# Kernel optimization log

Hardware: AMD Instinct MI355X
Metric: run time of the kernel (lower is better)

## Reference

```python
import jax, jax.numpy as jnp
import numpy as np
import math
from jax import lax

ALPHA = 2.0          # surrogate.ATan(alpha=2.0)
TAU = 2.0
BASE_THR = 1.0
ADAPT = 0.1          # adaptation_strength
TARGET_RATE = 0.1
DECAY = math.exp(-1.0 / TAU)
N_HEAD = 4

@jax.custom_vjp
def atan_spike(x):
    # forward: Heaviside; backward: ATan surrogate gradient
    return (x >= 0).astype(x.dtype)

def _atan_fwd(x):
    return atan_spike(x), x

def _atan_bwd(x, g):
    return (g * (ALPHA / 2.0) / (1.0 + (math.pi / 2.0 * ALPHA * x) ** 2),)

atan_spike.defvjp(_atan_fwd, _atan_bwd)

def lif_step(x, v_mem, thr):
    # AdaptiveLIFNeuron.forward
    v_pot = v_mem * DECAY + x
    spike = atan_spike(v_pot - thr)
    sd = lax.stop_gradient(spike)
    v_new = v_pot * (1.0 - sd)                               # spike.detach()
    thr_new = thr + ADAPT * (sd.mean(axis=(0, 1)) - TARGET_RATE)  # no_grad buffer update
    return spike, v_new, thr_new

def setup_inputs() -> dict:
    key = jax.random.key(0)
    ks = jax.random.split(key, 12)
    B, T, S, dm, ds = 4, 96, 128, 512, 256
    W = 0.02  # scale weights so per-step activations stay numerically sane
    return {
        'x':  jax.random.normal(ks[0], (B, T, S, dm), jnp.float32),
        'A':  jax.random.normal(ks[1], (ds, ds), jnp.float32) * W,
        'C':  jax.random.normal(ks[2], (dm, ds), jnp.float32) * W,
        'D':  jax.random.normal(ks[3], (dm, dm), jnp.float32) * W,
        'Wq': jax.random.normal(ks[4], (ds, ds), jnp.float32) * W,
        'bq': jax.random.normal(ks[5], (ds,), jnp.float32) * W,
        'Wk': jax.random.normal(ks[6], (ds, dm), jnp.float32) * W,
        'bk': jax.random.normal(ks[7], (ds,), jnp.float32) * W,
        'Wv': jax.random.normal(ks[8], (ds, dm), jnp.float32) * W,
        'bv': jax.random.normal(ks[9], (ds,), jnp.float32) * W,
        'Wo': jax.random.normal(ks[10], (ds, ds), jnp.float32) * W,
        'bo': jax.random.normal(ks[11], (ds,), jnp.float32) * W,
    }

def _forward(x, A, C, D, Wq, bq, Wk, bk, Wv, bv, Wo, bo):
    B, T, S, dm = x.shape
    ds = A.shape[0]
    H = N_HEAD
    dh = ds // H
    BS = B * S
    scale = 1.0 / math.sqrt(dh)

    h0 = jnp.zeros((B, S, ds), x.dtype)
    sv0 = jnp.zeros((B, S, ds), x.dtype)
    ov0 = jnp.zeros((B, S, dm), x.dtype)
    ts0 = jnp.full((ds,), BASE_THR, x.dtype)
    to0 = jnp.full((dm,), BASE_THR, x.dtype)

    def step(carry, x_t):
        h, sv, ov, ts, to = carry
        st = h @ A.T  # state transition [B,S,ds]

        def active(_):
            q = (h @ Wq.T + bq).reshape(BS, H, dh)
            k = (x_t @ Wk.T + bk).reshape(BS, H, dh)
            v = (x_t @ Wv.T + bv).reshape(BS, H, dh)
            # attention over all B*S tokens jointly, per head: [H, BS, BS]
            w = jax.nn.softmax(jnp.einsum('qhd,khd->hqk', q, k) * scale, axis=-1)
            av = jnp.einsum('hqk,khd->qhd', w, v).reshape(B, S, ds)
            gi = av @ Wo.T + bo
            h2, sv2, ts2 = lif_step(st + gi, sv, ts)
            out_up = h2 @ C.T + x_t @ D.T
            os_, ov2, to2 = lif_step(out_up, ov, to)
            return (h2, sv2, ov2, ts2, to2, os_)

        def inactive(_):
            h2, sv2, ts2 = lif_step(st, sv, ts)
            return (h2, sv2, ov, ts2, to, jnp.zeros_like(x_t))

        h2, sv2, ov2, ts2, to2, os_ = lax.cond(jnp.any(x_t > 0), active, inactive, None)
        return (h2, sv2, ov2, ts2, to2), os_

    xs = jnp.swapaxes(x, 0, 1)  # [T,B,S,dm]
    _, outs = lax.scan(step, (h0, sv0, ov0, ts0, to0), xs)
    return jnp.swapaxes(outs, 0, 1)  # [B,T,S,dm]

def reference(x, A, C, D, Wq, bq, Wk, bk, Wv, bv, Wo, bo):
    return _forward(x, A, C, D, Wq, bq, Wk, bk, Wv, bv, Wo, bo)
```

## Files before the change

### kernel.cpp

```cpp
#include <hip/hip_runtime.h>
#include <math.h>

#define TT   96
#define SSS  128
#define DMM  512
#define DSS  256
#define BSS  512
#define NBLK 128
#define NTHR 1024
#define DECAYF 0.6065306597126334f
#define SMEM_BYTES 135712

static constexpr size_t OFS_K      = 0;
static constexpr size_t OFS_V      = 12582912;
static constexpr size_t OFS_XD     = 25165824;
static constexpr size_t OFS_AT     = 50331648;
static constexpr size_t OFS_WQT    = 50397184;
static constexpr size_t OFS_WOT    = 50462720;
static constexpr size_t OFS_CT     = 50528256;
static constexpr size_t OFS_TPART  = 50659328;
static constexpr size_t OFS_TOPART = 50671616;
static constexpr size_t OFS_FLAGS  = 50696192;
static constexpr size_t OFS_BAR    = 50696320;
static constexpr size_t WS_FLOATS  = 50696384;

#define L_PART 0
#define L_SW   16640
#define L_SH   24960
#define L_SSV  25984
#define L_SST  27008
#define L_SQV  28032
#define L_SAV  29056
#define L_SOV  30080
#define L_STS  32128
#define L_STO  32384
#define L_ACT  32896
#define L_NACT 33920

__device__ __forceinline__ void gridbar(int* bar, int* bok) {
  __syncthreads();
  if (threadIdx.x == 0) {
    if (*bok) {
      __threadfence();
      int* cnt = bar;
      int* gen = bar + 32;
      int g = __hip_atomic_load(gen, __ATOMIC_ACQUIRE, __HIP_MEMORY_SCOPE_AGENT);
      int a = __hip_atomic_fetch_add(cnt, 1, __ATOMIC_ACQ_REL, __HIP_MEMORY_SCOPE_AGENT);
      if (a == NBLK - 1) {
        __hip_atomic_store(cnt, 0, __ATOMIC_RELAXED, __HIP_MEMORY_SCOPE_AGENT);
        __hip_atomic_fetch_add(gen, 1, __ATOMIC_ACQ_REL, __HIP_MEMORY_SCOPE_AGENT);
      } else {
        int spin = 0;
        while (__hip_atomic_load(gen, __ATOMIC_ACQUIRE, __HIP_MEMORY_SCOPE_AGENT) == g) {
          __builtin_amdgcn_s_sleep(8);
          if (++spin > (1 << 22)) { *bok = 0; break; }
        }
      }
      __threadfence();
    }
  }
  __syncthreads();
}

extern "C" __global__ void __launch_bounds__(256)
zfill_kernel(float* __restrict__ out, int n) {
  int i = blockIdx.x * 256 + threadIdx.x;
  if (i < n) out[i] = 0.f;
}

extern "C" __global__ void __launch_bounds__(256)
flags_kernel(const float* __restrict__ x, int* __restrict__ flags) {
  __shared__ int f;
  if (threadIdx.x == 0) f = 0;
  __syncthreads();
  int t = blockIdx.x;
  int any = 0;
  for (int b = 0; b < 4; ++b) {
    const float4* base = (const float4*)(x + ((size_t)(b * TT + t) * SSS) * DMM);
    for (int i = threadIdx.x; i < 16384; i += 256) {
      float4 v = base[i];
      any |= (v.x > 0.f) | (v.y > 0.f) | (v.z > 0.f) | (v.w > 0.f);
    }
  }
  if (any) atomicOr(&f, 1);
  __syncthreads();
  if (threadIdx.x == 0) flags[t] = f;
}

extern "C" __global__ void __launch_bounds__(256)
tr_kernel(const float* __restrict__ A, const float* __restrict__ Wq,
          const float* __restrict__ Wo, const float* __restrict__ C,
          float* __restrict__ ws) {
  __shared__ float tile[32][33];
  int b = blockIdx.x;
  const float* src; float* dst; int RS, CS, tb;
  if (b < 64)       { src = A;  dst = ws + OFS_AT;  RS = 256; CS = 256; tb = b; }
  else if (b < 128) { src = Wq; dst = ws + OFS_WQT; RS = 256; CS = 256; tb = b - 64; }
  else if (b < 192) { src = Wo; dst = ws + OFS_WOT; RS = 256; CS = 256; tb = b - 128; }
  else              { src = C;  dst = ws + OFS_CT;  RS = 512; CS = 256; tb = b - 192; }
  int tpr = CS / 32;
  int trr = tb / tpr, tcc = tb % tpr;
  int r0 = trr * 32, c0 = tcc * 32;
  int tx = threadIdx.x & 31, ty = threadIdx.x >> 5;
  #pragma unroll
  for (int j = 0; j < 4; ++j)
    tile[ty + j * 8][tx] = src[(size_t)(r0 + ty + j * 8) * CS + c0 + tx];
  __syncthreads();
  #pragma unroll
  for (int j = 0; j < 4; ++j)
    dst[(size_t)(c0 + ty + j * 8) * RS + r0 + tx] = tile[tx][ty + j * 8];
}

extern "C" __global__ void __launch_bounds__(256)
pre_kernel(const float* __restrict__ x,
           const float* __restrict__ Wk, const float* __restrict__ bk,
           const float* __restrict__ Wv, const float* __restrict__ bv,
           const float* __restrict__ D,  float* __restrict__ ws) {
  __shared__ float As[32 * 68];
  __shared__ float Bs[32 * 68];
  int bid = blockIdx.x;
  int nt = bid & 15, mt = bid >> 4;
  int row0 = mt * 64, col0 = nt * 64;
  int tid = threadIdx.x;
  int trd = tid & 15, tc = tid >> 4;
  float acc[4][4] = {};
  for (int kk = 0; kk < 512; kk += 32) {
    __syncthreads();
    { int m = tid >> 2, ks = (tid & 3) * 8;
      const float* src = x + (size_t)(row0 + m) * 512 + kk + ks;
      float4 a = *(const float4*)(src);
      float4 b = *(const float4*)(src + 4);
      As[(ks + 0) * 68 + m] = a.x; As[(ks + 1) * 68 + m] = a.y;
      As[(ks + 2) * 68 + m] = a.z; As[(ks + 3) * 68 + m] = a.w;
      As[(ks + 4) * 68 + m] = b.x; As[(ks + 5) * 68 + m] = b.y;
      As[(ks + 6) * 68 + m] = b.z; As[(ks + 7) * 68 + m] = b.w; }
    { int n = tid >> 2, ks = (tid & 3) * 8;
      int gc = col0 + n;
      const float* wr = (gc < 256) ? (Wk + (size_t)gc * 512)
                      : (gc < 512) ? (Wv + (size_t)(gc - 256) * 512)
                                   : (D  + (size_t)(gc - 512) * 512);
      const float* src = wr + kk + ks;
      float4 a = *(const float4*)(src);
      float4 b = *(const float4*)(src + 4);
      Bs[(ks + 0) * 68 + n] = a.x; Bs[(ks + 1) * 68 + n] = a.y;
      Bs[(ks + 2) * 68 + n] = a.z; Bs[(ks + 3) * 68 + n] = a.w;
      Bs[(ks + 4) * 68 + n] = b.x; Bs[(ks + 5) * 68 + n] = b.y;
      Bs[(ks + 6) * 68 + n] = b.z; Bs[(ks + 7) * 68 + n] = b.w; }
    __syncthreads();
    #pragma unroll 8
    for (int k = 0; k < 32; ++k) {
      float4 a4 = *(const float4*)(As + k * 68 + trd * 4);
      float4 b4 = *(const float4*)(Bs + k * 68 + tc * 4);
      float am[4] = {a4.x, a4.y, a4.z, a4.w};
      float bn[4] = {b4.x, b4.y, b4.z, b4.w};
      #pragma unroll
      for (int i = 0; i < 4; ++i)
        #pragma unroll
        for (int j = 0; j < 4; ++j)
          acc[i][j] = fmaf(am[i], bn[j], acc[i][j]);
    }
  }
  for (int i = 0; i < 4; ++i) {
    int g = row0 + trd * 4 + i;
    int b = g / 12288, r1 = g % 12288;
    int t_ = r1 / 128, s_ = r1 % 128;
    size_t drow = (size_t)t_ * BSS + b * SSS + s_;
    int gc0 = col0 + tc * 4;
    float4 o = make_float4(acc[i][0], acc[i][1], acc[i][2], acc[i][3]);
    if (gc0 < 256) {
      o.x += bk[gc0]; o.y += bk[gc0 + 1]; o.z += bk[gc0 + 2]; o.w += bk[gc0 + 3];
      *(float4*)(ws + OFS_K + drow * DSS + gc0) = o;
    } else if (gc0 < 512) {
      int c = gc0 - 256;
      o.x += bv[c]; o.y += bv[c + 1]; o.z += bv[c + 2]; o.w += bv[c + 3];
      *(float4*)(ws + OFS_V + drow * DSS + c) = o;
    } else {
      *(float4*)(ws + OFS_XD + drow * DMM + (gc0 - 512)) = o;
    }
  }
}

extern "C" __global__ void __launch_bounds__(NTHR, 4)
seq_kernel(const float* __restrict__ bq, const float* __restrict__ bo,
           float* __restrict__ ws, float* __restrict__ out) {
  extern __shared__ float sm[];
  float* part = sm + L_PART;
  float* sw   = sm + L_SW;
  float* sh   = sm + L_SH;
  float* ssv  = sm + L_SSV;
  float* sst  = sm + L_SST;
  float* sqv  = sm + L_SQV;
  float* sav  = sm + L_SAV;
  float* sou  = sm + L_SQV;
  float* sov  = sm + L_SOV;
  float* sts  = sm + L_STS;
  float* sto  = sm + L_STO;
  int*   acts = (int*)(sm + L_ACT);
  int*   nact = (int*)(sm + L_NACT);
  int*   bok  = nact + 7;

  const float* At  = ws + OFS_AT;
  const float* Wqt = ws + OFS_WQT;
  const float* Wot = ws + OFS_WOT;
  const float* Ct  = ws + OFS_CT;
  const float* XD  = ws + OFS_XD;
  float* tpart  = ws + OFS_TPART;
  float* topart = ws + OFS_TOPART;
  const int* flags = (const int*)(ws + OFS_FLAGS);
  int* bar = (int*)(ws + OFS_BAR);

  const int tid = threadIdx.x;
  const int bid = blockIdx.x;

  sh[tid] = 0.f;
  ssv[tid] = 0.f;
  sov[tid] = 0.f; sov[1024 + tid] = 0.f;
  if (tid < 256) sts[tid] = 1.f;
  if (tid < 512) sto[tid] = 1.f;
  if (tid == 0) *bok = 1;
  { size_t g0 = (size_t)bid * NTHR + tid;
    for (size_t i = g0; i < (size_t)36864; i += (size_t)NBLK * NTHR)
      tpart[i] = 0.f; }
  gridbar(bar, bok);

  for (int t = 0; t < TT; ++t) {
    const int fl = flags[t];
    const int tb3 = t % 3;
    const float* Kt = ws + OFS_K + (size_t)t * BSS * DSS;
    const float* Vt = ws + OFS_V + (size_t)t * BSS * DSS;

    if (tid < 256) {
      int r = tid >> 6, lane = tid & 63;
      int base = 0;
      for (int seg = 0; seg < 4; ++seg) {
        int k = seg * 64 + lane;
        bool p = sh[r * 256 + k] > 0.5f;
        unsigned long long m = __ballot(p);
        int pre = __popcll(m & ((1ull << lane) - 1ull));
        if (p) acts[r * 256 + base + pre] = k;
        base += __popcll(m);
      }
      if (lane == 0) nact[r] = base;
    }
    __syncthreads();

    {
      int r = tid >> 8, c = tid & 255;
      int n = nact[r];
      const int* al = acts + r * 256;
      float aS = 0.f, aQ = 0.f;
      if (fl) {
        for (int i = 0; i < n; ++i) {
          int k = al[i];
          aS += At[(size_t)k * 256 + c];
          aQ += Wqt[(size_t)k * 256 + c];
        }
        sqv[r * 256 + c] = aQ + bq[c];
      } else {
        for (int i = 0; i < n; ++i) aS += At[(size_t)(al[i]) * 256 + c];
      }
      sst[r * 256 + c] = aS;
    }
    __syncthreads();

    if (fl) {
      int kl = tid >> 5, dsg = tid & 31;
      float4 qa[4], qb[4];
      #pragma unroll
      for (int r = 0; r < 4; ++r) {
        qa[r] = *(const float4*)(sqv + r * 256 + dsg * 8);
        qb[r] = *(const float4*)(sqv + r * 256 + dsg * 8 + 4);
      }
      for (int kb = 0; kb < 16; ++kb) {
        int key = kb * 32 + kl;
        const float4* kp = (const float4*)(Kt + (size_t)key * 256 + dsg * 8);
        float4 k0 = kp[0], k1 = kp[1];
        float p[4];
        #pragma unroll
        for (int r = 0; r < 4; ++r) {
          float s = 0.f;
          s = fmaf(k0.x, qa[r].x, s); s = fmaf(k0.y, qa[r].y, s);
          s = fmaf(k0.z, qa[r].z, s); s = fmaf(k0.w, qa[r].w, s);
          s = fmaf(k1.x, qb[r].x, s); s = fmaf(k1.y, qb[r].y, s);
          s = fmaf(k1.z, qb[r].z, s); s = fmaf(k1.w, qb[r].w, s);
          p[r] = s;
        }
        *(float4*)(part + (size_t)(kl * 33 + dsg) * 4) = make_float4(p[0], p[1], p[2], p[3]);
        __syncthreads();
        if (tid < 512) {
          int r2 = tid >> 7, hd = (tid >> 5) & 3, kl2 = tid & 31;
          float s = 0.f;
          #pragma unroll
          for (int d8 = 0; d8 < 8; ++d8)
            s += part[(size_t)(kl2 * 33 + hd * 8 + d8) * 4 + r2];
          sw[(r2 * 4 + hd) * 520 + kb * 32 + kl2] = s * 0.125f;
        }
        __syncthreads();
      }

      {
        int w = tid >> 6, lane = tid & 63;
        float* row = sw + w * 520;
        float4 v0 = ((const float4*)row)[lane * 2];
        float4 v1 = ((const float4*)row)[lane * 2 + 1];
        float m = fmaxf(fmaxf(fmaxf(v0.x, v0.y), fmaxf(v0.z, v0.w)),
                        fmaxf(fmaxf(v1.x, v1.y), fmaxf(v1.z, v1.w)));
        for (int o = 32; o > 0; o >>= 1) m = fmaxf(m, __shfl_xor(m, o));
        v0.x = expf(v0.x - m); v0.y = expf(v0.y - m); v0.z = expf(v0.z - m); v0.w = expf(v0.w - m);
        v1.x = expf(v1.x - m); v1.y = expf(v1.y - m); v1.z = expf(v1.z - m); v1.w = expf(v1.w - m);
        float s = v0.x + v0.y + v0.z + v0.w + v1.x + v1.y + v1.z + v1.w;
        for (int o = 32; o > 0; o >>= 1) s += __shfl_xor(s, o);
        float inv = 1.f / s;
        v0.x *= inv; v0.y *= inv; v0.z *= inv; v0.w *= inv;
        v1.x *= inv; v1.y *= inv; v1.z *= inv; v1.w *= inv;
        ((float4*)row)[lane * 2] = v0; ((float4*)row)[lane * 2 + 1] = v1;
      }
      __syncthreads();

      {
        int kg = tid >> 6, dq = tid & 63;
        int hd = dq >> 4;
        float4 acc[4];
        #pragma unroll
        for (int r = 0; r < 4; ++r) acc[r] = make_float4(0.f, 0.f, 0.f, 0.f);
        for (int kb = 0; kb < 8; ++kb) {
          #pragma unroll
          for (int i = 0; i < 4; ++i) {
            int key = kb * 64 + kg * 4 + i;
            float4 v = *(const float4*)(Vt + (size_t)key * 256 + dq * 4);
            #pragma unroll
            for (int r = 0; r < 4; ++r) {
              float wv = sw[(r * 4 + hd) * 520 + key];
              acc[r].x = fmaf(wv, v.x, acc[r].x);
              acc[r].y = fmaf(wv, v.y, acc[r].y);
              acc[r].z = fmaf(wv, v.z, acc[r].z);
              acc[r].w = fmaf(wv, v.w, acc[r].w);
            }
          }
        }
        #pragma unroll
        for (int r = 0; r < 4; ++r)
          *(float4*)(part + (size_t)((kg * 4 + r) * 64 + dq) * 4) = acc[r];
      }
      __syncthreads();
      {
        int row = tid >> 8, dd = tid & 255;
        float s = 0.f;
        #pragma unroll
        for (int kg = 0; kg < 16; ++kg)
          s += part[(size_t)kg * 1024 + row * 256 + dd];
        sav[row * 256 + dd] = s;
      }
      __syncthreads();
    }

    {
      int r = tid >> 8, c = tid & 255;
      float gi = 0.f;
      if (fl) {
        int ks4 = (tid >> 6) & 3, cq = tid & 63;
        float4 a = make_float4(0.f, 0.f, 0.f, 0.f);
        const float* avr = sav + r * 256;
        for (int k = ks4 * 64; k < ks4 * 64 + 64; ++k) {
          float avv = avr[k];
          float4 wo = *(const float4*)(Wot + (size_t)k * 256 + cq * 4);
          a.x = fmaf(avv, wo.x, a.x); a.y = fmaf(avv, wo.y, a.y);
          a.z = fmaf(avv, wo.z, a.z); a.w = fmaf(avv, wo.w, a.w);
        }
        *(float4*)(part + (size_t)((r * 4 + ks4) * 64 + cq) * 4) = a;
        __syncthreads();
        gi = (((part[(size_t)(r * 4 + 0) * 256 + c]
              + part[(size_t)(r * 4 + 1) * 256 + c])
              + part[(size_t)(r * 4 + 2) * 256 + c])
              + part[(size_t)(r * 4 + 3) * 256 + c]) + bo[c];
      }
      float in1 = sst[r * 256 + c] + gi;
      float vp = ssv[r * 256 + c] * DECAYF + in1;
      float sp = (vp >= sts[c]) ? 1.f : 0.f;
      ssv[r * 256 + c] = vp * (1.f - sp);
      sh[r * 256 + c] = sp;
    }
    __syncthreads();
    if (tid < 256) {
      float s = sh[tid] + sh[256 + tid] + sh[512 + tid] + sh[768 + tid];
      atomicAdd(tpart + ((size_t)tb3 * 16 + (bid & 15)) * 256 + tid, s);
    }

    if (fl) {
      if (tid < 256) {
        int r = tid >> 6, lane = tid & 63;
        int base = 0;
        for (int seg = 0; seg < 4; ++seg) {
          int k = seg * 64 + lane;
          bool p = sh[r * 256 + k] > 0.5f;
          unsigned long long m = __ballot(p);
          int pre = __popcll(m & ((1ull << lane) - 1ull));
          if (p) acts[r * 256 + base + pre] = k;
          base += __popcll(m);
        }
        if (lane == 0) nact[r] = base;
      }
      __syncthreads();
      {
        int r = tid >> 8, c2 = tid & 255, m0 = c2 * 2;
        int grow = bid * 4 + r;
        int n = nact[r];
        const int* al = acts + r * 256;
        float a0 = 0.f, a1 = 0.f;
        for (int i = 0; i < n; ++i) {
          int k = al[i];
          float2 cv = *(const float2*)(Ct + (size_t)k * 512 + m0);
          a0 += cv.x; a1 += cv.y;
        }
        float2 xd = *(const float2*)(XD + ((size_t)t * 512 + grow) * 512 + m0);
        float up0 = a0 + xd.x, up1 = a1 + xd.y;
        float vp0 = sov[r * 512 + m0] * DECAYF + up0;
        float vp1 = sov[r * 512 + m0 + 1] * DECAYF + up1;
        float s0 = (vp0 >= sto[m0]) ? 1.f : 0.f;
        float s1 = (vp1 >= sto[m0 + 1]) ? 1.f : 0.f;
        sov[r * 512 + m0] = vp0 * (1.f - s0);
        sov[r * 512 + m0 + 1] = vp1 * (1.f - s1);
        sou[r * 512 + m0] = s0; sou[r * 512 + m0 + 1] = s1;
        int b = grow >> 7, sI = grow & 127;
        float2 o2; o2.x = s0; o2.y = s1;
        *(float2*)(out + (((size_t)b * TT + t) * SSS + sI) * DMM + m0) = o2;
      }
      __syncthreads();
      if (tid < 512) {
        float s = sou[tid] + sou[512 + tid] + sou[1024 + tid] + sou[1536 + tid];
        atomicAdd(topart + ((size_t)tb3 * 16 + (bid & 15)) * 512 + tid, s);
      }
    } else {
      int r = tid >> 8, c2 = tid & 255, m0 = c2 * 2;
      int grow = bid * 4 + r;
      int b = grow >> 7, sI = grow & 127;
      float2 z; z.x = 0.f; z.y = 0.f;
      *(float2*)(out + (((size_t)b * TT + t) * SSS + sI) * DMM + m0) = z;
    }

    gridbar(bar, bok);

    if (tid < 256) {
      float s = 0.f;
      const float* tp = tpart + (size_t)tb3 * 4096;
      #pragma unroll
      for (int b2 = 0; b2 < 16; ++b2) s += tp[b2 * 256 + tid];
      sts[tid] += 0.1f * (s * (1.f / 512.f) - 0.1f);
    } else if (tid >= 512 && fl) {
      int c = tid - 512;
      const float* tp = topart + (size_t)tb3 * 8192;
      float s = 0.f;
      #pragma unroll
      for (int b2 = 0; b2 < 16; ++b2) s += tp[b2 * 512 + c];
      sto[c] += 0.1f * (s * (1.f / 512.f) - 0.1f);
    }
    {
      int bz = (t + 2) % 3;
      size_t g = (size_t)bid * NTHR + tid;
      if (g < 4096) tpart[(size_t)bz * 4096 + g] = 0.f;
      else if (g < 12288) topart[(size_t)bz * 8192 + (g - 4096)] = 0.f;
    }
    __syncthreads();
  }
}

extern "C" void kernel_launch(void* const* d_in, const int* in_sizes, int n_in,
                              void* d_out, int out_size, void* d_ws, size_t ws_size,
                              hipStream_t stream) {
  const float* x  = (const float*)d_in[0];
  const float* Aw = (const float*)d_in[1];
  const float* Cw = (const float*)d_in[2];
  const float* Dw = (const float*)d_in[3];
  const float* Wq = (const float*)d_in[4];
  const float* bq = (const float*)d_in[5];
  const float* Wk = (const float*)d_in[6];
  const float* bk = (const float*)d_in[7];
  const float* Wv = (const float*)d_in[8];
  const float* bv = (const float*)d_in[9];
  const float* Wo = (const float*)d_in[10];
  const float* bo = (const float*)d_in[11];
  float* ws  = (float*)d_ws;
  float* out = (float*)d_out;

  if (ws_size < WS_FLOATS * sizeof(float)) {
    hipLaunchKernelGGL(zfill_kernel, dim3((out_size + 255) / 256), dim3(256), 0, stream,
                       out, out_size);
    return;
  }

  hipMemsetAsync((void*)(ws + OFS_BAR), 0, 256, stream);
  hipLaunchKernelGGL(flags_kernel, dim3(TT), dim3(256), 0, stream, x, (int*)(ws + OFS_FLAGS));
  hipLaunchKernelGGL(tr_kernel, dim3(320), dim3(256), 0, stream, Aw, Wq, Wo, Cw, ws);
  hipLaunchKernelGGL(pre_kernel, dim3(12288), dim3(256), 0, stream, x, Wk, bk, Wv, bv, Dw, ws);

  hipFuncSetAttribute((const void*)seq_kernel, hipFuncAttributeMaxDynamicSharedMemorySize, SMEM_BYTES);
  void* kargs[] = { (void*)&bq, (void*)&bo, (void*)&ws, (void*)&out };
  hipLaunchCooperativeKernel((void*)seq_kernel, dim3(NBLK), dim3(NTHR), kargs, SMEM_BYTES, stream);
}
```

Baseline: 10.22 ms.

## Use relaxed atomics in grid barrier and restructure QK score computation per key

The grid barrier drops acquire/release fences in favour of relaxed agent-scope atomics plus a vmcnt wait, and spins with a shorter sleep. The cross-block partial sums are now read and written through relaxed atomics so they stay coherent without full fences. The QK score loop no longer runs 16 rounds of partial writes to shared memory, each followed by two block-wide syncs. Instead each thread computes full head dot products for one key and one half of the head dimension, and reads q from shared memory. This removes many __syncthreads, but the relaxed memory ordering on the barrier could be fragile.

```diff
diff --git a/kernel.cpp b/kernel.cpp
--- a/kernel.cpp
+++ b/kernel.cpp
@@ -10,6 +10,10 @@
 #define NTHR 1024
 #define DECAYF 0.6065306597126334f
 #define SMEM_BYTES 135712
+
+#define AT_ADD(p, v) __hip_atomic_fetch_add((p), (v), __ATOMIC_RELAXED, __HIP_MEMORY_SCOPE_AGENT)
+#define AT_ST(p, v)  __hip_atomic_store((p), (v), __ATOMIC_RELAXED, __HIP_MEMORY_SCOPE_AGENT)
+#define AT_LD(p)     __hip_atomic_load((p), __ATOMIC_RELAXED, __HIP_MEMORY_SCOPE_AGENT)
 
 static constexpr size_t OFS_K      = 0;
 static constexpr size_t OFS_V      = 12582912;
@@ -39,25 +43,23 @@
 
 __device__ __forceinline__ void gridbar(int* bar, int* bok) {
   __syncthreads();
-  if (threadIdx.x == 0) {
-    if (*bok) {
-      __threadfence();
-      int* cnt = bar;
-      int* gen = bar + 32;
-      int g = __hip_atomic_load(gen, __ATOMIC_ACQUIRE, __HIP_MEMORY_SCOPE_AGENT);
-      int a = __hip_atomic_fetch_add(cnt, 1, __ATOMIC_ACQ_REL, __HIP_MEMORY_SCOPE_AGENT);
-      if (a == NBLK - 1) {
-        __hip_atomic_store(cnt, 0, __ATOMIC_RELAXED, __HIP_MEMORY_SCOPE_AGENT);
-        __hip_atomic_fetch_add(gen, 1, __ATOMIC_ACQ_REL, __HIP_MEMORY_SCOPE_AGENT);
-      } else {
-        int spin = 0;
-        while (__hip_atomic_load(gen, __ATOMIC_ACQUIRE, __HIP_MEMORY_SCOPE_AGENT) == g) {
-          __builtin_amdgcn_s_sleep(8);
-          if (++spin > (1 << 22)) { *bok = 0; break; }
-        }
-      }
-      __threadfence();
-    }
+  if (threadIdx.x == 0 && *bok) {
+    asm volatile("s_waitcnt vmcnt(0)" ::: "memory");
+    int* cnt = bar;
+    int* gen = bar + 32;
+    int g = AT_LD(gen);
+    int a = AT_ADD(cnt, 1);
+    if (a == NBLK - 1) {
+      AT_ST(cnt, 0);
+      AT_ADD(gen, 1);
+    } else {
+      int spin = 0;
+      while (AT_LD(gen) == g) {
+        __builtin_amdgcn_s_sleep(2);
+        if (++spin > (1 << 23)) { *bok = 0; break; }
+      }
+    }
+    __atomic_signal_fence(__ATOMIC_SEQ_CST);
   }
   __syncthreads();
 }
@@ -220,7 +222,7 @@
   if (tid == 0) *bok = 1;
   { size_t g0 = (size_t)bid * NTHR + tid;
     for (size_t i = g0; i < (size_t)36864; i += (size_t)NBLK * NTHR)
-      tpart[i] = 0.f; }
+      AT_ST(&tpart[i], 0.f); }
   gridbar(bar, bok);
 
   for (int t = 0; t < TT; ++t) {
@@ -264,39 +266,45 @@
     __syncthreads();
 
     if (fl) {
-      int kl = tid >> 5, dsg = tid & 31;
-      float4 qa[4], qb[4];
-      #pragma unroll
-      for (int r = 0; r < 4; ++r) {
-        qa[r] = *(const float4*)(sqv + r * 256 + dsg * 8);
-        qb[r] = *(const float4*)(sqv + r * 256 + dsg * 8 + 4);
-      }
-      for (int kb = 0; kb < 16; ++kb) {
-        int key = kb * 32 + kl;
-        const float4* kp = (const float4*)(Kt + (size_t)key * 256 + dsg * 8);
-        float4 k0 = kp[0], k1 = kp[1];
-        float p[4];
+      {
+        int hp  = tid >> 9;
+        int key = tid & 511;
+        const float4* kp = (const float4*)(Kt + (size_t)key * 256 + hp * 128);
+        float a0[4] = {0.f, 0.f, 0.f, 0.f};
+        float a1[4] = {0.f, 0.f, 0.f, 0.f};
+        int db = hp * 128;
+        #pragma unroll 4
+        for (int i = 0; i < 16; ++i) {
+          float4 kv4 = kp[i];
+          #pragma unroll
+          for (int r = 0; r < 4; ++r) {
+            float4 q4 = *(const float4*)(sqv + r * 256 + db + i * 4);
+            a0[r] = fmaf(kv4.x, q4.x, a0[r]);
+            a0[r] = fmaf(kv4.y, q4.y, a0[r]);
+            a0[r] = fmaf(kv4.z, q4.z, a0[r]);
+            a0[r] = fmaf(kv4.w, q4.w, a0[r]);
+          }
+        }
+        #pragma unroll 4
+        for (int i = 16; i < 32; ++i) {
+          float4 kv4 = kp[i];
+          #pragma unroll
+          for (int r = 0; r < 4; ++r) {
+            float4 q4 = *(const float4*)(sqv + r * 256 + db + i * 4);
+            a1[r] = fmaf(kv4.x, q4.x, a1[r]);
+            a1[r] = fmaf(kv4.y, q4.y, a1[r]);
+            a1[r] = fmaf(kv4.z, q4.z, a1[r]);
+            a1[r] = fmaf(kv4.w, q4.w, a1[r]);
+          }
+        }
+        int hd0 = hp * 2;
         #pragma unroll
         for (int r = 0; r < 4; ++r) {
-          float s = 0.f;
-          s = fmaf(k0.x, qa[r].x, s); s = fmaf(k0.y, qa[r].y, s);
-          s = fmaf(k0.z, qa[r].z, s); s = fmaf(k0.w, qa[r].w, s);
-          s = fmaf(k1.x, qb[r].x, s); s = fmaf(k1.y, qb[r].y, s);
-          s = fmaf(k1.z, qb[r].z, s); s = fmaf(k1.w, qb[r].w, s);
-          p[r] = s;
-        }
-        *(float4*)(part + (size_t)(kl * 33 + dsg) * 4) = make_float4(p[0], p[1], p[2], p[3]);
-        __syncthreads();
-        if (tid < 512) {
-          int r2 = tid >> 7, hd = (tid >> 5) & 3, kl2 = tid & 31;
-          float s = 0.f;
-          #pragma unroll
-          for (int d8 = 0; d8 < 8; ++d8)
-            s += part[(size_t)(kl2 * 33 + hd * 8 + d8) * 4 + r2];
-          sw[(r2 * 4 + hd) * 520 + kb * 32 + kl2] = s * 0.125f;
-        }
-        __syncthreads();
-      }
+          sw[(r * 4 + hd0) * 520 + key]     = a0[r] * 0.125f;
+          sw[(r * 4 + hd0 + 1) * 520 + key] = a1[r] * 0.125f;
+        }
+      }
+      __syncthreads();
 
       {
         int w = tid >> 6, lane = tid & 63;
@@ -383,7 +391,7 @@
     __syncthreads();
     if (tid < 256) {
       float s = sh[tid] + sh[256 + tid] + sh[512 + tid] + sh[768 + tid];
-      atomicAdd(tpart + ((size_t)tb3 * 16 + (bid & 15)) * 256 + tid, s);
+      AT_ADD(tpart + ((size_t)tb3 * 16 + (bid & 15)) * 256 + tid, s);
     }
 
     if (fl) {
@@ -428,7 +436,7 @@
       __syncthreads();
       if (tid < 512) {
         float s = sou[tid] + sou[512 + tid] + sou[1024 + tid] + sou[1536 + tid];
-        atomicAdd(topart + ((size_t)tb3 * 16 + (bid & 15)) * 512 + tid, s);
+        AT_ADD(topart + ((size_t)tb3 * 16 + (bid & 15)) * 512 + tid, s);
       }
     } else {
       int r = tid >> 8, c2 = tid & 255, m0 = c2 * 2;
@@ -441,24 +449,24 @@
     gridbar(bar, bok);
 
     if (tid < 256) {
+      const float* tp = tpart + (size_t)tb3 * 4096 + tid;
       float s = 0.f;
-      const float* tp = tpart + (size_t)tb3 * 4096;
       #pragma unroll
-      for (int b2 = 0; b2 < 16; ++b2) s += tp[b2 * 256 + tid];
+      for (int b2 = 0; b2 < 16; ++b2) s += AT_LD(tp + b2 * 256);
       sts[tid] += 0.1f * (s * (1.f / 512.f) - 0.1f);
     } else if (tid >= 512 && fl) {
       int c = tid - 512;
-      const float* tp = topart + (size_t)tb3 * 8192;
+      const float* tp = topart + (size_t)tb3 * 8192 + c;
       float s = 0.f;
       #pragma unroll
-      for (int b2 = 0; b2 < 16; ++b2) s += tp[b2 * 512 + c];
+      for (int b2 = 0; b2 < 16; ++b2) s += AT_LD(tp + b2 * 512);
       sto[c] += 0.1f * (s * (1.f / 512.f) - 0.1f);
     }
     {
       int bz = (t + 2) % 3;
       size_t g = (size_t)bid * NTHR + tid;
-      if (g < 4096) tpart[(size_t)bz * 4096 + g] = 0.f;
-      else if (g < 12288) topart[(size_t)bz * 8192 + (g - 4096)] = 0.f;
+      if (g < 4096) AT_ST(&tpart[(size_t)bz * 4096 + g], 0.f);
+      else if (g < 12288) AT_ST(&topart[(size_t)bz * 8192 + (g - 4096)], 0.f);
     }
     __syncthreads();
   }
```

Result: faster. 8.982 ms (-12.1%).

## Split sequential kernel across more blocks with arrival-counter sync and transposed K

Applied to the files above, without the earlier changes.

Doubles the persistent block count and halves the threads per block, so each block handles two tokens instead of four. The full grid barrier is replaced by a monotonic arrival counter, and the threshold-stat reduction is deferred until just before the LIF update, so the attention work of the next step can overlap with the wait. K is stored transposed per timestep, which lets each thread compute whole key scores without a shared-memory reduction. The V and Wo stages are reorganized to match. Risks include more atomic contention on single counters and strided scattered stores of K in the pre-kernel.

```diff
diff --git a/kernel.cpp b/kernel.cpp
--- a/kernel.cpp
+++ b/kernel.cpp
@@ -6,61 +6,26 @@
 #define DMM  512
 #define DSS  256
 #define BSS  512
-#define NBLK 128
-#define NTHR 1024
+#define NBLK 256
+#define NTHR 512
 #define DECAYF 0.6065306597126334f
-#define SMEM_BYTES 135712
-
-static constexpr size_t OFS_K      = 0;
-static constexpr size_t OFS_V      = 12582912;
-static constexpr size_t OFS_XD     = 25165824;
-static constexpr size_t OFS_AT     = 50331648;
-static constexpr size_t OFS_WQT    = 50397184;
-static constexpr size_t OFS_WOT    = 50462720;
-static constexpr size_t OFS_CT     = 50528256;
-static constexpr size_t OFS_TPART  = 50659328;
-static constexpr size_t OFS_TOPART = 50671616;
-static constexpr size_t OFS_FLAGS  = 50696192;
-static constexpr size_t OFS_BAR    = 50696320;
-static constexpr size_t WS_FLOATS  = 50696384;
-
-#define L_PART 0
-#define L_SW   16640
-#define L_SH   24960
-#define L_SSV  25984
-#define L_SST  27008
-#define L_SQV  28032
-#define L_SAV  29056
-#define L_SOV  30080
-#define L_STS  32128
-#define L_STO  32384
-#define L_ACT  32896
-#define L_NACT 33920
-
-__device__ __forceinline__ void gridbar(int* bar, int* bok) {
-  __syncthreads();
-  if (threadIdx.x == 0) {
-    if (*bok) {
-      __threadfence();
-      int* cnt = bar;
-      int* gen = bar + 32;
-      int g = __hip_atomic_load(gen, __ATOMIC_ACQUIRE, __HIP_MEMORY_SCOPE_AGENT);
-      int a = __hip_atomic_fetch_add(cnt, 1, __ATOMIC_ACQ_REL, __HIP_MEMORY_SCOPE_AGENT);
-      if (a == NBLK - 1) {
-        __hip_atomic_store(cnt, 0, __ATOMIC_RELAXED, __HIP_MEMORY_SCOPE_AGENT);
-        __hip_atomic_fetch_add(gen, 1, __ATOMIC_ACQ_REL, __HIP_MEMORY_SCOPE_AGENT);
-      } else {
-        int spin = 0;
-        while (__hip_atomic_load(gen, __ATOMIC_ACQUIRE, __HIP_MEMORY_SCOPE_AGENT) == g) {
-          __builtin_amdgcn_s_sleep(8);
-          if (++spin > (1 << 22)) { *bok = 0; break; }
-        }
-      }
-      __threadfence();
-    }
-  }
-  __syncthreads();
-}
+
+#define AT_ADD(p, v) __hip_atomic_fetch_add((p), (v), __ATOMIC_RELAXED, __HIP_MEMORY_SCOPE_AGENT)
+#define AT_ST(p, v)  __hip_atomic_store((p), (v), __ATOMIC_RELAXED, __HIP_MEMORY_SCOPE_AGENT)
+#define AT_LD(p)     __hip_atomic_load((p), __ATOMIC_RELAXED, __HIP_MEMORY_SCOPE_AGENT)
+
+static constexpr size_t OFS_KT    = 0;
+static constexpr size_t OFS_V     = 12582912;
+static constexpr size_t OFS_XD    = 25165824;
+static constexpr size_t OFS_AT    = 50331648;
+static constexpr size_t OFS_WQT   = 50397184;
+static constexpr size_t OFS_WOT   = 50462720;
+static constexpr size_t OFS_CT    = 50528256;
+static constexpr size_t OFS_TP    = 50659328;
+static constexpr size_t OFS_TOP   = 50660096;
+static constexpr size_t OFS_FLAGS = 50661632;
+static constexpr size_t OFS_ARR   = 50661760;
+static constexpr size_t WS_FLOATS = 50661824;
 
 extern "C" __global__ void __launch_bounds__(256)
 zfill_kernel(float* __restrict__ out, int n) {
@@ -164,12 +129,15 @@
     int g = row0 + trd * 4 + i;
     int b = g / 12288, r1 = g % 12288;
     int t_ = r1 / 128, s_ = r1 % 128;
-    size_t drow = (size_t)t_ * BSS + b * SSS + s_;
+    int tokidx = b * SSS + s_;
+    size_t drow = (size_t)t_ * BSS + tokidx;
     int gc0 = col0 + tc * 4;
     float4 o = make_float4(acc[i][0], acc[i][1], acc[i][2], acc[i][3]);
     if (gc0 < 256) {
-      o.x += bk[gc0]; o.y += bk[gc0 + 1]; o.z += bk[gc0 + 2]; o.w += bk[gc0 + 3];
-      *(float4*)(ws + OFS_K + drow * DSS + gc0) = o;
+      float vals[4] = {o.x + bk[gc0], o.y + bk[gc0 + 1], o.z + bk[gc0 + 2], o.w + bk[gc0 + 3]};
+      #pragma unroll
+      for (int j = 0; j < 4; ++j)
+        ws[OFS_KT + (size_t)t_ * 131072 + (size_t)(gc0 + j) * 512 + tokidx] = vals[j];
     } else if (gc0 < 512) {
       int c = gc0 - 256;
       o.x += bv[c]; o.y += bv[c + 1]; o.z += bv[c + 2]; o.w += bv[c + 3];
@@ -180,56 +148,51 @@
   }
 }
 
-extern "C" __global__ void __launch_bounds__(NTHR, 4)
+extern "C" __global__ void __launch_bounds__(NTHR)
 seq_kernel(const float* __restrict__ bq, const float* __restrict__ bo,
            float* __restrict__ ws, float* __restrict__ out) {
-  extern __shared__ float sm[];
-  float* part = sm + L_PART;
-  float* sw   = sm + L_SW;
-  float* sh   = sm + L_SH;
-  float* ssv  = sm + L_SSV;
-  float* sst  = sm + L_SST;
-  float* sqv  = sm + L_SQV;
-  float* sav  = sm + L_SAV;
-  float* sou  = sm + L_SQV;
-  float* sov  = sm + L_SOV;
-  float* sts  = sm + L_STS;
-  float* sto  = sm + L_STO;
-  int*   acts = (int*)(sm + L_ACT);
-  int*   nact = (int*)(sm + L_NACT);
-  int*   bok  = nact + 7;
+  __shared__ float part[4096];
+  __shared__ float sw[8 * 520];
+  __shared__ float sh[512];
+  __shared__ float ssv[512];
+  __shared__ float sst[512];
+  __shared__ float squ[1024];
+  __shared__ float sov[1024];
+  __shared__ float sts[DSS];
+  __shared__ float sto[DMM];
+  __shared__ int   acts[512];
+  __shared__ int   nact2[2];
+  __shared__ int   bok;
+
+  float* sqv = squ;
+  float* sav = squ + 512;
+  float* sou = squ;
 
   const float* At  = ws + OFS_AT;
   const float* Wqt = ws + OFS_WQT;
   const float* Wot = ws + OFS_WOT;
   const float* Ct  = ws + OFS_CT;
   const float* XD  = ws + OFS_XD;
-  float* tpart  = ws + OFS_TPART;
-  float* topart = ws + OFS_TOPART;
+  float* tp  = ws + OFS_TP;
+  float* top = ws + OFS_TOP;
   const int* flags = (const int*)(ws + OFS_FLAGS);
-  int* bar = (int*)(ws + OFS_BAR);
+  int* arr = (int*)(ws + OFS_ARR);
 
   const int tid = threadIdx.x;
   const int bid = blockIdx.x;
 
   sh[tid] = 0.f;
   ssv[tid] = 0.f;
-  sov[tid] = 0.f; sov[1024 + tid] = 0.f;
+  sov[tid] = 0.f; sov[512 + tid] = 0.f;
   if (tid < 256) sts[tid] = 1.f;
-  if (tid < 512) sto[tid] = 1.f;
-  if (tid == 0) *bok = 1;
-  { size_t g0 = (size_t)bid * NTHR + tid;
-    for (size_t i = g0; i < (size_t)36864; i += (size_t)NBLK * NTHR)
-      tpart[i] = 0.f; }
-  gridbar(bar, bok);
+  sto[tid] = 1.f;
+  if (tid == 0) bok = 1;
+  __syncthreads();
 
   for (int t = 0; t < TT; ++t) {
     const int fl = flags[t];
-    const int tb3 = t % 3;
-    const float* Kt = ws + OFS_K + (size_t)t * BSS * DSS;
-    const float* Vt = ws + OFS_V + (size_t)t * BSS * DSS;
-
-    if (tid < 256) {
+
+    if (tid < 128) {
       int r = tid >> 6, lane = tid & 63;
       int base = 0;
       for (int seg = 0; seg < 4; ++seg) {
@@ -240,13 +203,13 @@
         if (p) acts[r * 256 + base + pre] = k;
         base += __popcll(m);
       }
-      if (lane == 0) nact[r] = base;
+      if (lane == 0) nact2[r] = base;
     }
     __syncthreads();
 
     {
       int r = tid >> 8, c = tid & 255;
-      int n = nact[r];
+      int n = nact2[r];
       const int* al = acts + r * 256;
       float aS = 0.f, aQ = 0.f;
       if (fl) {
@@ -264,39 +227,22 @@
     __syncthreads();
 
     if (fl) {
-      int kl = tid >> 5, dsg = tid & 31;
-      float4 qa[4], qb[4];
-      #pragma unroll
-      for (int r = 0; r < 4; ++r) {
-        qa[r] = *(const float4*)(sqv + r * 256 + dsg * 8);
-        qb[r] = *(const float4*)(sqv + r * 256 + dsg * 8 + 4);
-      }
-      for (int kb = 0; kb < 16; ++kb) {
-        int key = kb * 32 + kl;
-        const float4* kp = (const float4*)(Kt + (size_t)key * 256 + dsg * 8);
-        float4 k0 = kp[0], k1 = kp[1];
-        float p[4];
+      {
+        const float* ktb = ws + OFS_KT + (size_t)t * 131072 + tid;
         #pragma unroll
-        for (int r = 0; r < 4; ++r) {
-          float s = 0.f;
-          s = fmaf(k0.x, qa[r].x, s); s = fmaf(k0.y, qa[r].y, s);
-          s = fmaf(k0.z, qa[r].z, s); s = fmaf(k0.w, qa[r].w, s);
-          s = fmaf(k1.x, qb[r].x, s); s = fmaf(k1.y, qb[r].y, s);
-          s = fmaf(k1.z, qb[r].z, s); s = fmaf(k1.w, qb[r].w, s);
-          p[r] = s;
+        for (int hd = 0; hd < 4; ++hd) {
+          float a0 = 0.f, a1 = 0.f;
+          #pragma unroll 16
+          for (int j = 0; j < 64; ++j) {
+            float kv = ktb[(size_t)(hd * 64 + j) * 512];
+            a0 = fmaf(kv, sqv[hd * 64 + j], a0);
+            a1 = fmaf(kv, sqv[256 + hd * 64 + j], a1);
+          }
+          sw[hd * 520 + tid]       = a0 * 0.125f;
+          sw[(4 + hd) * 520 + tid] = a1 * 0.125f;
         }
-        *(float4*)(part + (size_t)(kl * 33 + dsg) * 4) = make_float4(p[0], p[1], p[2], p[3]);
-        __syncthreads();
-        if (tid < 512) {
-          int r2 = tid >> 7, hd = (tid >> 5) & 3, kl2 = tid & 31;
-          float s = 0.f;
-          #pragma unroll
-          for (int d8 = 0; d8 < 8; ++d8)
-            s += part[(size_t)(kl2 * 33 + hd * 8 + d8) * 4 + r2];
-          sw[(r2 * 4 + hd) * 520 + kb * 32 + kl2] = s * 0.125f;
-        }
-        __syncthreads();
-      }
+      }
+      __syncthreads();
 
       {
         int w = tid >> 6, lane = tid & 63;
@@ -318,62 +264,85 @@
       __syncthreads();
 
       {
-        int kg = tid >> 6, dq = tid & 63;
-        int hd = dq >> 4;
-        float4 acc[4];
-        #pragma unroll
-        for (int r = 0; r < 4; ++r) acc[r] = make_float4(0.f, 0.f, 0.f, 0.f);
-        for (int kb = 0; kb < 8; ++kb) {
-          #pragma unroll
-          for (int i = 0; i < 4; ++i) {
-            int key = kb * 64 + kg * 4 + i;
-            float4 v = *(const float4*)(Vt + (size_t)key * 256 + dq * 4);
-            #pragma unroll
-            for (int r = 0; r < 4; ++r) {
-              float wv = sw[(r * 4 + hd) * 520 + key];
-              acc[r].x = fmaf(wv, v.x, acc[r].x);
-              acc[r].y = fmaf(wv, v.y, acc[r].y);
-              acc[r].z = fmaf(wv, v.z, acc[r].z);
-              acc[r].w = fmaf(wv, v.w, acc[r].w);
-            }
-          }
+        int kg = tid >> 6, dq = tid & 63, hd = dq >> 4;
+        const float4* vp = (const float4*)(ws + OFS_V + (size_t)t * 131072) + dq;
+        float4 a0 = make_float4(0.f, 0.f, 0.f, 0.f);
+        float4 a1 = make_float4(0.f, 0.f, 0.f, 0.f);
+        for (int i = 0; i < 64; ++i) {
+          int key = kg * 64 + i;
+          float4 v = vp[(size_t)key * 64];
+          float w0 = sw[hd * 520 + key];
+          float w1 = sw[(4 + hd) * 520 + key];
+          a0.x = fmaf(w0, v.x, a0.x); a0.y = fmaf(w0, v.y, a0.y);
+          a0.z = fmaf(w0, v.z, a0.z); a0.w = fmaf(w0, v.w, a0.w);
+          a1.x = fmaf(w1, v.x, a1.x); a1.y = fmaf(w1, v.y, a1.y);
+          a1.z = fmaf(w1, v.z, a1.z); a1.w = fmaf(w1, v.w, a1.w);
         }
-        #pragma unroll
-        for (int r = 0; r < 4; ++r)
-          *(float4*)(part + (size_t)((kg * 4 + r) * 64 + dq) * 4) = acc[r];
+        *(float4*)(part + (kg * 2 + 0) * 256 + dq * 4) = a0;
+        *(float4*)(part + (kg * 2 + 1) * 256 + dq * 4) = a1;
       }
       __syncthreads();
       {
-        int row = tid >> 8, dd = tid & 255;
+        int r = tid >> 8, d = tid & 255;
         float s = 0.f;
         #pragma unroll
-        for (int kg = 0; kg < 16; ++kg)
-          s += part[(size_t)kg * 1024 + row * 256 + dd];
-        sav[row * 256 + dd] = s;
+        for (int kg = 0; kg < 8; ++kg) s += part[(kg * 2 + r) * 256 + d];
+        sav[r * 256 + d] = s;
+      }
+      __syncthreads();
+    }
+
+    float gi = 0.f;
+    if (fl) {
+      int r6 = tid >> 8, ks4 = (tid >> 6) & 3, cq = tid & 63;
+      float4 a = make_float4(0.f, 0.f, 0.f, 0.f);
+      const float* avr = sav + r6 * 256;
+      for (int k = ks4 * 64; k < ks4 * 64 + 64; ++k) {
+        float avv = avr[k];
+        float4 wo = *(const float4*)(Wot + (size_t)k * 256 + cq * 4);
+        a.x = fmaf(avv, wo.x, a.x); a.y = fmaf(avv, wo.y, a.y);
+        a.z = fmaf(avv, wo.z, a.z); a.w = fmaf(avv, wo.w, a.w);
+      }
+      *(float4*)(part + ((r6 * 4 + ks4) * 64 + cq) * 4) = a;
+      __syncthreads();
+      int r = tid >> 8, c = tid & 255;
+      gi = (((part[(r * 4 + 0) * 256 + c]
+            + part[(r * 4 + 1) * 256 + c])
+            + part[(r * 4 + 2) * 256 + c])
+            + part[(r * 4 + 3) * 256 + c]) + bo[c];
+    }
+
+    __syncthreads();
+    if (tid == 0 && t > 0 && bok) {
+      int target = t * NBLK;
+      int spin = 0;
+      while (AT_LD(arr) < target) {
+        if (spin < 256) __builtin_amdgcn_s_sleep(1);
+        else            __builtin_amdgcn_s_sleep(16);
+        if (++spin > (1 << 21)) { bok = 0; break; }
+      }
+    }
+    __syncthreads();
+    if (t > 0) {
+      int ps = (t - 1) % 3;
+      if (tid < 256) {
+        float s = AT_LD(tp + ps * 256 + tid);
+        sts[tid] += 0.1f * (s * (1.f / 512.f) - 0.1f);
+      }
+      if (flags[t - 1]) {
+        float s = AT_LD(top + ps * 512 + tid);
+        sto[tid] += 0.1f * (s * (1.f / 512.f) - 0.1f);
+      }
+      if (bid == 0) {
+        int zs = (t + 1) % 3;
+        if (tid < 256) AT_ST(tp + zs * 256 + tid, 0.f);
+        AT_ST(top + zs * 512 + tid, 0.f);
       }
       __syncthreads();
     }
 
     {
       int r = tid >> 8, c = tid & 255;
-      float gi = 0.f;
-      if (fl) {
-        int ks4 = (tid >> 6) & 3, cq = tid & 63;
-        float4 a = make_float4(0.f, 0.f, 0.f, 0.f);
-        const float* avr = sav + r * 256;
-        for (int k = ks4 * 64; k < ks4 * 64 + 64; ++k) {
-          float avv = avr[k];
-          float4 wo = *(const float4*)(Wot + (size_t)k * 256 + cq * 4);
-          a.x = fmaf(avv, wo.x, a.x); a.y = fmaf(avv, wo.y, a.y);
-          a.z = fmaf(avv, wo.z, a.z); a.w = fmaf(avv, wo.w, a.w);
-        }
-        *(float4*)(part + (size_t)((r * 4 + ks4) * 64 + cq) * 4) = a;
-        __syncthreads();
-        gi = (((part[(size_t)(r * 4 + 0) * 256 + c]
-              + part[(size_t)(r * 4 + 1) * 256 + c])
-              + part[(size_t)(r * 4 + 2) * 256 + c])
-              + part[(size_t)(r * 4 + 3) * 256 + c]) + bo[c];
-      }
       float in1 = sst[r * 256 + c] + gi;
       float vp = ssv[r * 256 + c] * DECAYF + in1;
       float sp = (vp >= sts[c]) ? 1.f : 0.f;
@@ -381,13 +350,10 @@
       sh[r * 256 + c] = sp;
     }
     __syncthreads();
-    if (tid < 256) {
-      float s = sh[tid] + sh[256 + tid] + sh[512 + tid] + sh[768 + tid];
-      atomicAdd(tpart + ((size_t)tb3 * 16 + (bid & 15)) * 256 + tid, s);
-    }
+    if (tid < 256) AT_ADD(tp + (t % 3) * 256 + tid, sh[tid] + sh[256 + tid]);
 
     if (fl) {
-      if (tid < 256) {
+      if (tid < 128) {
         int r = tid >> 6, lane = tid & 63;
         int base = 0;
         for (int seg = 0; seg < 4; ++seg) {
@@ -398,13 +364,13 @@
           if (p) acts[r * 256 + base + pre] = k;
           base += __popcll(m);
         }
-        if (lane == 0) nact[r] = base;
+        if (lane == 0) nact2[r] = base;
       }
       __syncthreads();
       {
         int r = tid >> 8, c2 = tid & 255, m0 = c2 * 2;
-        int grow = bid * 4 + r;
-        int n = nact[r];
+        int grow = bid * 2 + r;
+        int n = nact2[r];
         const int* al = acts + r * 256;
         float a0 = 0.f, a1 = 0.f;
         for (int i = 0; i < n; ++i) {
@@ -426,41 +392,20 @@
         *(float2*)(out + (((size_t)b * TT + t) * SSS + sI) * DMM + m0) = o2;
       }
       __syncthreads();
-      if (tid < 512) {
-        float s = sou[tid] + sou[512 + tid] + sou[1024 + tid] + sou[1536 + tid];
-        atomicAdd(topart + ((size_t)tb3 * 16 + (bid & 15)) * 512 + tid, s);
-      }
+      AT_ADD(top + (t % 3) * 512 + tid, sou[tid] + sou[512 + tid]);
     } else {
       int r = tid >> 8, c2 = tid & 255, m0 = c2 * 2;
-      int grow = bid * 4 + r;
+      int grow = bid * 2 + r;
       int b = grow >> 7, sI = grow & 127;
       float2 z; z.x = 0.f; z.y = 0.f;
       *(float2*)(out + (((size_t)b * TT + t) * SSS + sI) * DMM + m0) = z;
     }
 
-    gridbar(bar, bok);
-
-    if (tid < 256) {
-      float s = 0.f;
-      const float* tp = tpart + (size_t)tb3 * 4096;
-      #pragma unroll
-      for (int b2 = 0; b2 < 16; ++b2) s += tp[b2 * 256 + tid];
-      sts[tid] += 0.1f * (s * (1.f / 512.f) - 0.1f);
-    } else if (tid >= 512 && fl) {
-      int c = tid - 512;
-      const float* tp = topart + (size_t)tb3 * 8192;
-      float s = 0.f;
-      #pragma unroll
-      for (int b2 = 0; b2 < 16; ++b2) s += tp[b2 * 512 + c];
-      sto[c] += 0.1f * (s * (1.f / 512.f) - 0.1f);
-    }
-    {
-      int bz = (t + 2) % 3;
-      size_t g = (size_t)bid * NTHR + tid;
-      if (g < 4096) tpart[(size_t)bz * 4096 + g] = 0.f;
-      else if (g < 12288) topart[(size_t)bz * 8192 + (g - 4096)] = 0.f;
-    }
-    __syncthreads();
+    __syncthreads();
+    if (tid == 0) {
+      asm volatile("s_waitcnt vmcnt(0)" ::: "memory");
+      AT_ADD(arr, 1);
+    }
   }
 }
 
@@ -488,12 +433,11 @@
     return;
   }
 
-  hipMemsetAsync((void*)(ws + OFS_BAR), 0, 256, stream);
+  hipMemsetAsync((void*)(ws + OFS_TP), 0, (WS_FLOATS - OFS_TP) * sizeof(float), stream);
   hipLaunchKernelGGL(flags_kernel, dim3(TT), dim3(256), 0, stream, x, (int*)(ws + OFS_FLAGS));
   hipLaunchKernelGGL(tr_kernel, dim3(320), dim3(256), 0, stream, Aw, Wq, Wo, Cw, ws);
   hipLaunchKernelGGL(pre_kernel, dim3(12288), dim3(256), 0, stream, x, Wk, bk, Wv, bv, Dw, ws);
 
-  hipFuncSetAttribute((const void*)seq_kernel, hipFuncAttributeMaxDynamicSharedMemorySize, SMEM_BYTES);
   void* kargs[] = { (void*)&bq, (void*)&bo, (void*)&ws, (void*)&out };
-  hipLaunchCooperativeKernel((void*)seq_kernel, dim3(NBLK), dim3(NTHR), kargs, SMEM_BYTES, stream);
-}
+  hipLaunchCooperativeKernel((void*)seq_kernel, dim3(NBLK), dim3(NTHR), kargs, 0, stream);
+}
```

After: 11.16 ms. 1.09x slower.
